# Performance work log

Measured on AMD Instinct MI355X. Metric: run time of the kernel, lower is better.

The kernel has to match this reference:

```python
import jax, jax.numpy as jnp
import numpy as np

B, N, IN_DIM, H, D = 4, 2048, 128, 4, 64
NEG_SLOPE = 0.2
MASK_VAL = -1e9


def setup_inputs() -> dict:
    key = jax.random.key(0)
    k1, k2, k3, k4, k5 = jax.random.split(key, 5)
    x = jax.random.normal(k1, (B, N, IN_DIM), dtype=jnp.float32)
    adj = jax.random.randint(k2, (N, N), 0, 2, dtype=jnp.int32)
    W = jax.random.normal(k3, (H * D, IN_DIM), dtype=jnp.float32) * 0.05
    att_src = jax.random.normal(k4, (1, H, D), dtype=jnp.float32) * 0.05
    att_dst = jax.random.normal(k5, (1, H, D), dtype=jnp.float32) * 0.05
    return {"x": x, "adj": adj, "W": W, "att_src": att_src, "att_dst": att_dst}


def reference(x, adj, W, att_src, att_dst):
    # linear (no bias), torch layout: y = x @ W.T  -> [B,N,H*D]
    h = jnp.einsum('bni,oi->bno', x, W).reshape(B, N, H, D).transpose(0, 2, 1, 3)  # [B,H,N,D]
    e_src = jnp.einsum('bhnd,hd->bhn', h, att_src[0])  # [B,H,N]
    e_dst = jnp.einsum('bhnd,hd->bhn', h, att_dst[0])  # [B,H,N]
    # additive score: e[b,h,i,j] = leaky_relu(e_src[b,h,i] + e_dst[b,h,j])
    e = jax.nn.leaky_relu(e_src[..., :, None] + e_dst[..., None, :], NEG_SLOPE)  # [B,H,N,N]
    e = jnp.where(adj[None, None] <= 0, MASK_VAL, e)
    attn = jax.nn.softmax(e, axis=-1)  # dropout inactive (inference)
    out = jnp.einsum('bhij,bhjd->bhid', attn, h)  # [B,H,N,D]
    return out.transpose(0, 2, 1, 3).reshape(B, N, H * D)  # concat heads
```

## Files before the change

kernel.cpp:

```cpp
#include <hip/hip_runtime.h>


#define NDIM 2048
#define NEG_SLOPE 0.2f
#define LOG2E 1.4426950408889634f

typedef __bf16 bf16x8 __attribute__((ext_vector_type(8)));
typedef __bf16 bf16x4 __attribute__((ext_vector_type(4)));
typedef float  f32x4  __attribute__((ext_vector_type(4)));

#define LP 136

__device__ static inline void load_lds16(const void* g, void* l) {
    __builtin_amdgcn_global_load_lds(
        (const __attribute__((address_space(1))) unsigned*)g,
        (__attribute__((address_space(3))) unsigned*)l, 16, 0, 0);
}

__global__ __launch_bounds__(256) void gat_pre(
    const float* __restrict__ x, const int* __restrict__ adj,
    const float* __restrict__ W, const float* __restrict__ att_src,
    const float* __restrict__ att_dst, __bf16* __restrict__ h_t,
    float* __restrict__ es_ws, float* __restrict__ ed_ws,
    unsigned* __restrict__ bits)
{
    const int t = threadIdx.x;

    if (blockIdx.x >= 512) {
        const int q = (blockIdx.x - 512) * 256 + t;
        int4 a = ((const int4*)adj)[q];
        unsigned nib = (unsigned)(a.x > 0) | ((unsigned)(a.y > 0) << 1) |
                       ((unsigned)(a.z > 0) << 2) | ((unsigned)(a.w > 0) << 3);
        unsigned v = nib << ((t & 7) * 4);
        v |= __shfl_xor(v, 1, 64);
        v |= __shfl_xor(v, 2, 64);
        v |= __shfl_xor(v, 4, 64);
        if ((t & 7) == 0) bits[q >> 3] = v;
        return;
    }

    const int head = blockIdx.x & 3;
    const int n0g  = (blockIdx.x >> 2) * 64;
    const int b    = n0g >> 11;
    const int n0   = n0g & (NDIM - 1);
    const int bh   = b * 4 + head;

    __shared__ __align__(16) __bf16 Wl[64][LP];
    __shared__ __align__(16) __bf16 Xl[64][LP];

    #pragma unroll
    for (int i = 0; i < 8; ++i) {
        int idx = t + i * 256;
        int r = idx >> 5, c4 = idx & 31;
        float4 wv = *((const float4*)(W + (size_t)(head * 64 + r) * 128) + c4);
        bf16x4 bv;
        bv[0] = (__bf16)wv.x; bv[1] = (__bf16)wv.y; bv[2] = (__bf16)wv.z; bv[3] = (__bf16)wv.w;
        *(bf16x4*)&Wl[r][c4 * 4] = bv;
    }
    #pragma unroll
    for (int i = 0; i < 8; ++i) {
        int idx = t + i * 256;
        int r = idx >> 5, c4 = idx & 31;
        float4 xv = *((const float4*)(x + (size_t)(n0g + r) * 128) + c4);
        bf16x4 bv;
        bv[0] = (__bf16)xv.x; bv[1] = (__bf16)xv.y; bv[2] = (__bf16)xv.z; bv[3] = (__bf16)xv.w;
        *(bf16x4*)&Xl[r][c4 * 4] = bv;
    }
    __syncthreads();

    const int lane = t & 63, w = t >> 6;
    const int m = lane & 15, q4 = lane >> 4;

    bf16x8 bfr[4];
    #pragma unroll
    for (int ks = 0; ks < 4; ++ks)
        bfr[ks] = *(const bf16x8*)&Xl[w * 16 + m][ks * 32 + q4 * 8];

    f32x4 acc[4];
    #pragma unroll
    for (int c = 0; c < 4; ++c) acc[c] = (f32x4){0.f, 0.f, 0.f, 0.f};

    #pragma unroll
    for (int ct = 0; ct < 4; ++ct) {
        #pragma unroll
        for (int ks = 0; ks < 4; ++ks) {
            bf16x8 afr = *(const bf16x8*)&Wl[ct * 16 + m][ks * 32 + q4 * 8];
            acc[ct] = __builtin_amdgcn_mfma_f32_16x16x32_bf16(afr, bfr[ks], acc[ct], 0, 0, 0);
        }
    }

    const int nloc = n0 + w * 16 + m;
    float esA = 0.f, edA = 0.f;
    #pragma unroll
    for (int ct = 0; ct < 4; ++ct) {
        float4 aS = *(const float4*)(att_src + head * 64 + ct * 16 + q4 * 4);
        float4 aD = *(const float4*)(att_dst + head * 64 + ct * 16 + q4 * 4);
        #pragma unroll
        for (int r = 0; r < 4; ++r) {
            float v = acc[ct][r];
            int   d = ct * 16 + q4 * 4 + r;
            h_t[(size_t)(bh * 64 + d) * NDIM + nloc] = (__bf16)v;
            esA += v * ((const float*)&aS)[r];
            edA += v * ((const float*)&aD)[r];
        }
    }
    esA += __shfl_xor(esA, 16, 64); esA += __shfl_xor(esA, 32, 64);
    edA += __shfl_xor(edA, 16, 64); edA += __shfl_xor(edA, 32, 64);
    if (lane < 16) {
        es_ws[bh * NDIM + nloc] = esA * LOG2E;
        ed_ws[bh * NDIM + nloc] = edA * LOG2E;
    }
}

__global__ __launch_bounds__(512, 4) void gat_attn(
    const unsigned long long* __restrict__ bits, const __bf16* __restrict__ h_t,
    const float* __restrict__ es_ws, const float* __restrict__ ed_ws,
    float* __restrict__ out)
{
    const int blk = blockIdx.x;
    const int bh  = blk & 15;
    const int i0  = (blk >> 4) * 64;
    const int t   = threadIdx.x;
    const int lane = t & 63, w = t >> 6;
    const int gJ = w >> 2, wl = w & 3;
    const int m = lane & 15, q4 = lane >> 4;

    __shared__ __align__(16) __bf16 Hl[2][2][64][64];

    const int r0 = wl * 16 + (lane >> 3);
    const int r1 = r0 + 8;
    const int c8 = lane & 7;
    const size_t jbase = (size_t)gJ * 1024;
    const __bf16* g0 = h_t + ((size_t)(bh * 64 + r0)) * NDIM + jbase + ((c8 ^ (r0 & 7)) * 8);
    const __bf16* g1 = h_t + ((size_t)(bh * 64 + r1)) * NDIM + jbase + ((c8 ^ (r1 & 7)) * 8);
    __bf16* l0a = &Hl[gJ][0][r0][c8 * 8];
    __bf16* l0b = &Hl[gJ][0][r1][c8 * 8];
    __bf16* l1a = &Hl[gJ][1][r0][c8 * 8];
    __bf16* l1b = &Hl[gJ][1][r1][c8 * 8];

    const float es2 = es_ws[bh * NDIM + i0 + wl * 16 + m];
    const unsigned long long* brow = bits + (size_t)(i0 + wl * 16 + m) * 32 + gJ * 16;
    const float* edp = ed_ws + bh * NDIM + jbase + q4 * 8;

    load_lds16(g0, l0a);
    load_lds16(g1, l0b);
    float eb[2][16];
    unsigned long long bwb[2];
    #pragma unroll
    for (int g4 = 0; g4 < 4; ++g4)
        *(float4*)&eb[0][g4 * 4] = *(const float4*)(edp + (g4 >> 1) * 32 + (g4 & 1) * 4);
    bwb[0] = brow[0];

    f32x4 acc[4], accl;
    #pragma unroll
    for (int c = 0; c < 4; ++c) acc[c] = (f32x4){0.f, 0.f, 0.f, 0.f};
    accl = (f32x4){0.f, 0.f, 0.f, 0.f};
    bf16x8 ones;
    #pragma unroll
    for (int jj = 0; jj < 8; ++jj) ones[jj] = (__bf16)1.0f;
    const int sw = m & 7;

    __syncthreads();

#define STEP(ITJ, P)                                                            \
    {                                                                           \
        const int itj = (ITJ);                                                  \
        if (itj < 15) {                                                         \
            load_lds16(g0 + (itj + 1) * 64, (P) ? l0a : l1a);                   \
            load_lds16(g1 + (itj + 1) * 64, (P) ? l0b : l1b);                   \
            const float* ep = edp + (itj + 1) * 64;                             \
            _Pragma("unroll")                                                   \
            for (int g4 = 0; g4 < 4; ++g4)                                      \
                *(float4*)&eb[(P) ^ 1][g4 * 4] =                                \
                    *(const float4*)(ep + (g4 >> 1) * 32 + (g4 & 1) * 4);       \
            bwb[(P) ^ 1] = brow[itj + 1];                                       \
        }                                                                       \
        bf16x8 af[2];                                                           \
        _Pragma("unroll")                                                       \
        for (int ks = 0; ks < 2; ++ks) {                                        \
            unsigned bm = (unsigned)(bwb[P] >> (ks * 32 + q4 * 8)) & 0xFFu;     \
            _Pragma("unroll")                                                   \
            for (int jj = 0; jj < 8; ++jj) {                                    \
                float s = es2 + eb[P][ks * 8 + jj];                             \
                s = fmaxf(s, NEG_SLOPE * s);                                    \
                s = ((bm >> jj) & 1u) ? s : -10000.0f;                          \
                af[ks][jj] = (__bf16)__builtin_amdgcn_exp2f(s);                 \
            }                                                                   \
        }                                                                       \
        _Pragma("unroll")                                                       \
        for (int ks = 0; ks < 2; ++ks) {                                        \
            accl = __builtin_amdgcn_mfma_f32_16x16x32_bf16(af[ks], ones, accl, 0, 0, 0); \
            _Pragma("unroll")                                                   \
            for (int ct = 0; ct < 4; ++ct) {                                    \
                bf16x8 bfr = *(const bf16x8*)&Hl[gJ][P][ct * 16 + m][((ks * 4 + q4) ^ sw) * 8]; \
                acc[ct] = __builtin_amdgcn_mfma_f32_16x16x32_bf16(af[ks], bfr, acc[ct], 0, 0, 0); \
            }                                                                   \
        }                                                                       \
        __syncthreads();                                                        \
    }

    for (int it2 = 0; it2 < 8; ++it2) {
        STEP(it2 * 2, 0);
        STEP(it2 * 2 + 1, 1);
    }
#undef STEP

    float* sc = (float*)&Hl[0][0][0][0];
    const int sidx = (wl * 64 + lane) * 24;
    if (w >= 4) {
        #pragma unroll
        for (int ct = 0; ct < 4; ++ct) *(f32x4*)&sc[sidx + ct * 4] = acc[ct];
        *(f32x4*)&sc[sidx + 16] = accl;
    }
    __syncthreads();
    if (w < 4) {
        #pragma unroll
        for (int ct = 0; ct < 4; ++ct) {
            f32x4 o = *(const f32x4*)&sc[sidx + ct * 4];
            acc[ct] = acc[ct] + o;
        }
        f32x4 lo = *(const f32x4*)&sc[sidx + 16];
        accl = accl + lo;

        float invr[4];
        #pragma unroll
        for (int r = 0; r < 4; ++r) invr[r] = 1.f / accl[r];

        const int b = bh >> 2, head = bh & 3;
        float* ob = out + ((size_t)(b * NDIM + i0 + wl * 16)) * 256 + head * 64;
        #pragma unroll
        for (int ct = 0; ct < 4; ++ct) {
            #pragma unroll
            for (int r = 0; r < 4; ++r) {
                ob[(size_t)(q4 * 4 + r) * 256 + ct * 16 + m] = acc[ct][r] * invr[r];
            }
        }
    }
}

extern "C" void kernel_launch(void* const* d_in, const int* in_sizes, int n_in,
                              void* d_out, int out_size, void* d_ws, size_t ws_size,
                              hipStream_t stream) {
    const float* x       = (const float*)d_in[0];
    const int*   adj     = (const int*)d_in[1];
    const float* W       = (const float*)d_in[2];
    const float* att_src = (const float*)d_in[3];
    const float* att_dst = (const float*)d_in[4];
    float* out = (float*)d_out;

    __bf16*   h_t   = (__bf16*)d_ws;
    float*    es_ws = (float*)((char*)d_ws + (size_t)4 * 1024 * 1024);
    float*    ed_ws = es_ws + 16 * NDIM;
    unsigned* bitsp = (unsigned*)(ed_ws + 16 * NDIM);

    gat_pre<<<4608, 256, 0, stream>>>(x, adj, W, att_src, att_dst, h_t, es_ws, ed_ws, bitsp);
    gat_attn<<<512, 512, 0, stream>>>((const unsigned long long*)bitsp, h_t, es_ws, ed_ws, out);
}
```

Baseline: 106.3 us.

## Triple-buffer LDS tiles with prefetch distance two and partial vmcnt waits

Grows the shared-memory H tile buffer from two to three stages so global-to-LDS loads are issued two iterations ahead. The full __syncthreads per step is replaced with an explicit s_waitcnt vmcnt plus s_barrier, so each step waits only for the tile it needs and later loads stay in flight. It also raises wave priority around the MFMA block. This adds 16KB of LDS per block, which may reduce occupancy at 4 blocks per CU, and the hand-counted vmcnt values must match the exact number of outstanding loads.

```diff
diff --git a/kernel.cpp b/kernel.cpp
--- a/kernel.cpp
+++ b/kernel.cpp
@@ -125,7 +125,7 @@
     const int gJ = w >> 2, wl = w & 3;
     const int m = lane & 15, q4 = lane >> 4;
 
-    __shared__ __align__(16) __bf16 Hl[2][2][64][64];
+    __shared__ __align__(16) __bf16 Hl[2][3][64][64];
 
     const int r0 = wl * 16 + (lane >> 3);
     const int r1 = r0 + 8;
@@ -137,13 +137,17 @@
     __bf16* l0b = &Hl[gJ][0][r1][c8 * 8];
     __bf16* l1a = &Hl[gJ][1][r0][c8 * 8];
     __bf16* l1b = &Hl[gJ][1][r1][c8 * 8];
+    __bf16* l2a = &Hl[gJ][2][r0][c8 * 8];
+    __bf16* l2b = &Hl[gJ][2][r1][c8 * 8];
 
     const float es2 = es_ws[bh * NDIM + i0 + wl * 16 + m];
     const unsigned long long* brow = bits + (size_t)(i0 + wl * 16 + m) * 32 + gJ * 16;
     const float* edp = ed_ws + bh * NDIM + jbase + q4 * 8;
 
-    load_lds16(g0, l0a);
-    load_lds16(g1, l0b);
+    load_lds16(g0,      l0a);
+    load_lds16(g1,      l0b);
+    load_lds16(g0 + 64, l1a);
+    load_lds16(g1 + 64, l1b);
     float eb[2][16];
     unsigned long long bwb[2];
     #pragma unroll
@@ -160,20 +164,24 @@
     for (int jj = 0; jj < 8; ++jj) ones[jj] = (__bf16)1.0f;
     const int sw = m & 7;
 
-    __syncthreads();
-
-#define STEP(ITJ, P)                                                            \
+    asm volatile("s_waitcnt vmcnt(7)" ::: "memory");
+    __builtin_amdgcn_s_barrier();
+    __builtin_amdgcn_sched_barrier(0);
+
+#define STEP(ITJ, P, RB, DA, DB, MODE)                                          \
     {                                                                           \
         const int itj = (ITJ);                                                  \
-        if (itj < 15) {                                                         \
-            load_lds16(g0 + (itj + 1) * 64, (P) ? l0a : l1a);                   \
-            load_lds16(g1 + (itj + 1) * 64, (P) ? l0b : l1b);                   \
+        if ((MODE) <= 1) {                                                      \
             const float* ep = edp + (itj + 1) * 64;                             \
             _Pragma("unroll")                                                   \
             for (int g4 = 0; g4 < 4; ++g4)                                      \
                 *(float4*)&eb[(P) ^ 1][g4 * 4] =                                \
                     *(const float4*)(ep + (g4 >> 1) * 32 + (g4 & 1) * 4);       \
             bwb[(P) ^ 1] = brow[itj + 1];                                       \
+        }                                                                       \
+        if ((MODE) == 0) {                                                      \
+            load_lds16(g0 + (itj + 2) * 64, (DA));                              \
+            load_lds16(g1 + (itj + 2) * 64, (DB));                              \
         }                                                                       \
         bf16x8 af[2];                                                           \
         _Pragma("unroll")                                                       \
@@ -187,23 +195,41 @@
                 af[ks][jj] = (__bf16)__builtin_amdgcn_exp2f(s);                 \
             }                                                                   \
         }                                                                       \
+        __builtin_amdgcn_s_setprio(1);                                          \
         _Pragma("unroll")                                                       \
         for (int ks = 0; ks < 2; ++ks) {                                        \
             accl = __builtin_amdgcn_mfma_f32_16x16x32_bf16(af[ks], ones, accl, 0, 0, 0); \
             _Pragma("unroll")                                                   \
             for (int ct = 0; ct < 4; ++ct) {                                    \
-                bf16x8 bfr = *(const bf16x8*)&Hl[gJ][P][ct * 16 + m][((ks * 4 + q4) ^ sw) * 8]; \
+                bf16x8 bfr = *(const bf16x8*)&Hl[gJ][RB][ct * 16 + m][((ks * 4 + q4) ^ sw) * 8]; \
                 acc[ct] = __builtin_amdgcn_mfma_f32_16x16x32_bf16(af[ks], bfr, acc[ct], 0, 0, 0); \
             }                                                                   \
         }                                                                       \
-        __syncthreads();                                                        \
-    }
-
-    for (int it2 = 0; it2 < 8; ++it2) {
-        STEP(it2 * 2, 0);
-        STEP(it2 * 2 + 1, 1);
-    }
+        __builtin_amdgcn_s_setprio(0);                                          \
+        if ((MODE) == 0) { asm volatile("s_waitcnt vmcnt(7)" ::: "memory"); }   \
+        else if ((MODE) == 1) { asm volatile("s_waitcnt vmcnt(5)" ::: "memory"); } \
+        if ((MODE) <= 1) {                                                      \
+            __builtin_amdgcn_s_barrier();                                       \
+            __builtin_amdgcn_sched_barrier(0);                                  \
+        }                                                                       \
+    }
+
+    for (int it6 = 0; it6 < 2; ++it6) {
+        const int s0 = it6 * 6;
+        STEP(s0 + 0, 0, 0, l2a, l2b, 0)
+        STEP(s0 + 1, 1, 1, l0a, l0b, 0)
+        STEP(s0 + 2, 0, 2, l1a, l1b, 0)
+        STEP(s0 + 3, 1, 0, l2a, l2b, 0)
+        STEP(s0 + 4, 0, 1, l0a, l0b, 0)
+        STEP(s0 + 5, 1, 2, l1a, l1b, 0)
+    }
+    STEP(12, 0, 0, l2a, l2b, 0)
+    STEP(13, 1, 1, l0a, l0b, 0)
+    STEP(14, 0, 2, l0a, l0b, 1)
+    STEP(15, 1, 0, l0a, l0b, 2)
 #undef STEP
+
+    __syncthreads();
 
     float* sc = (float*)&Hl[0][0][0][0];
     const int sidx = (wl * 64 + lane) * 24;
```

After: 107.7 us. About the same (+1.3%).

## Factor exp of leaky-relu score into precomputed per-node exponentials

Applied to the files above, without the earlier changes.

Uses exp2(leaky(a+b)) = max(exp2(a)exp2(b), exp2(0.2a)exp2(0.2b)), so the pre kernel stores exp2(s) and exp2(0.2s) pairs for the source and destination scores. The attention inner loop then does two multiplies, a max and a bitmask AND instead of an add, leaky-relu, select and a transcendental exp per element. The destination-score prefetch no longer uses a double buffer and is loaded inside each step, twice as wide. This drops the max-free softmax's safety margin: large scores can overflow or underflow the products, and the loads may now stall each step.

```diff
diff --git a/kernel.cpp b/kernel.cpp
--- a/kernel.cpp
+++ b/kernel.cpp
@@ -2,7 +2,6 @@
 
 
 #define NDIM 2048
-#define NEG_SLOPE 0.2f
 #define LOG2E 1.4426950408889634f
 
 typedef __bf16 bf16x8 __attribute__((ext_vector_type(8)));
@@ -107,8 +106,14 @@
     esA += __shfl_xor(esA, 16, 64); esA += __shfl_xor(esA, 32, 64);
     edA += __shfl_xor(edA, 16, 64); edA += __shfl_xor(edA, 32, 64);
     if (lane < 16) {
-        es_ws[bh * NDIM + nloc] = esA * LOG2E;
-        ed_ws[bh * NDIM + nloc] = edA * LOG2E;
+        float s2 = esA * LOG2E, d2 = edA * LOG2E;
+        float2 ev, dv;
+        ev.x = __builtin_amdgcn_exp2f(s2);
+        ev.y = __builtin_amdgcn_exp2f(0.2f * s2);
+        dv.x = __builtin_amdgcn_exp2f(d2);
+        dv.y = __builtin_amdgcn_exp2f(0.2f * d2);
+        ((float2*)es_ws)[(size_t)bh * NDIM + nloc] = ev;
+        ((float2*)ed_ws)[(size_t)bh * NDIM + nloc] = dv;
     }
 }
 
@@ -138,17 +143,14 @@
     __bf16* l1a = &Hl[gJ][1][r0][c8 * 8];
     __bf16* l1b = &Hl[gJ][1][r1][c8 * 8];
 
-    const float es2 = es_ws[bh * NDIM + i0 + wl * 16 + m];
+    const float2 eg = ((const float2*)es_ws)[(size_t)bh * NDIM + i0 + wl * 16 + m];
+    const float egx = eg.x, egy = eg.y;
     const unsigned long long* brow = bits + (size_t)(i0 + wl * 16 + m) * 32 + gJ * 16;
-    const float* edp = ed_ws + bh * NDIM + jbase + q4 * 8;
+    const float* edf = (const float*)(((const float2*)ed_ws) + (size_t)bh * NDIM + jbase + q4 * 8);
 
     load_lds16(g0, l0a);
     load_lds16(g1, l0b);
-    float eb[2][16];
     unsigned long long bwb[2];
-    #pragma unroll
-    for (int g4 = 0; g4 < 4; ++g4)
-        *(float4*)&eb[0][g4 * 4] = *(const float4*)(edp + (g4 >> 1) * 32 + (g4 & 1) * 4);
     bwb[0] = brow[0];
 
     f32x4 acc[4], accl;
@@ -165,14 +167,17 @@
 #define STEP(ITJ, P)                                                            \
     {                                                                           \
         const int itj = (ITJ);                                                  \
+        float fh[32];                                                           \
+        {                                                                       \
+            const float* fp = edf + (size_t)itj * 128;                          \
+            _Pragma("unroll")                                                   \
+            for (int g4 = 0; g4 < 8; ++g4)                                      \
+                *(float4*)&fh[g4 * 4] =                                         \
+                    *(const float4*)(fp + (g4 >> 2) * 64 + (g4 & 3) * 4);       \
+        }                                                                       \
         if (itj < 15) {                                                         \
             load_lds16(g0 + (itj + 1) * 64, (P) ? l0a : l1a);                   \
             load_lds16(g1 + (itj + 1) * 64, (P) ? l0b : l1b);                   \
-            const float* ep = edp + (itj + 1) * 64;                             \
-            _Pragma("unroll")                                                   \
-            for (int g4 = 0; g4 < 4; ++g4)                                      \
-                *(float4*)&eb[(P) ^ 1][g4 * 4] =                                \
-                    *(const float4*)(ep + (g4 >> 1) * 32 + (g4 & 1) * 4);       \
             bwb[(P) ^ 1] = brow[itj + 1];                                       \
         }                                                                       \
         bf16x8 af[2];                                                           \
@@ -181,10 +186,12 @@
             unsigned bm = (unsigned)(bwb[P] >> (ks * 32 + q4 * 8)) & 0xFFu;     \
             _Pragma("unroll")                                                   \
             for (int jj = 0; jj < 8; ++jj) {                                    \
-                float s = es2 + eb[P][ks * 8 + jj];                             \
-                s = fmaxf(s, NEG_SLOPE * s);                                    \
-                s = ((bm >> jj) & 1u) ? s : -10000.0f;                          \
-                af[ks][jj] = (__bf16)__builtin_amdgcn_exp2f(s);                 \
+                float t1 = egx * fh[ks * 16 + jj * 2];                          \
+                float t2 = egy * fh[ks * 16 + jj * 2 + 1];                      \
+                float p = fmaxf(t1, t2);                                        \
+                int mk = ((int)(bm << (31 - jj))) >> 31;                        \
+                p = __int_as_float(__float_as_int(p) & mk);                     \
+                af[ks][jj] = (__bf16)p;                                         \
             }                                                                   \
         }                                                                       \
         _Pragma("unroll")                                                       \
@@ -250,8 +257,8 @@
 
     __bf16*   h_t   = (__bf16*)d_ws;
     float*    es_ws = (float*)((char*)d_ws + (size_t)4 * 1024 * 1024);
-    float*    ed_ws = es_ws + 16 * NDIM;
-    unsigned* bitsp = (unsigned*)(ed_ws + 16 * NDIM);
+    float*    ed_ws = es_ws + (size_t)16 * NDIM * 2;
+    unsigned* bitsp = (unsigned*)(ed_ws + (size_t)16 * NDIM * 2);
 
     gat_pre<<<4608, 256, 0, stream>>>(x, adj, W, att_src, att_dst, h_t, es_ws, ed_ws, bitsp);
     gat_attn<<<512, 512, 0, stream>>>((const unsigned long long*)bitsp, h_t, es_ws, ed_ws, out);
```

New measurement: 114.6 us. 7.8% more time.
